# Kernel tuning notes

Hardware: AMD Instinct MI355X
Metric: run time of the kernel (lower is better)

## Reference

```python
import jax, jax.numpy as jnp
import numpy as np

DIM = 512
HEADS = 16
DIM_HEAD = 64
INNER = HEADS * DIM_HEAD
MAX_T = 32
BASE = 10000.0


def rotate_half(t):
    t1, t2 = jnp.split(t, 2, axis=-1)
    return jnp.concatenate((-t2, t1), axis=-1)


def setup_inputs() -> dict:
    key = jax.random.key(0)
    ks = jax.random.split(key, 12)
    B, T, S = 2, 16, 128
    x = jax.random.normal(ks[0], (B, T, S, DIM), dtype=jnp.float32)
    y = jax.random.normal(ks[1], (B, T, S, DIM), dtype=jnp.float32)
    temporal_mask = jax.random.randint(ks[2], (B, T, T), 0, 2).astype(jnp.int32)
    sc = 1.0 / np.sqrt(DIM)
    Wq = jax.random.normal(ks[3], (DIM, INNER), dtype=jnp.float32) * sc
    Wk = jax.random.normal(ks[4], (DIM, INNER), dtype=jnp.float32) * sc
    Wv = jax.random.normal(ks[5], (DIM, INNER), dtype=jnp.float32) * sc
    Wo = jax.random.normal(ks[6], (INNER, DIM), dtype=jnp.float32) / np.sqrt(INNER)
    bo = jnp.zeros((DIM,), dtype=jnp.float32)
    pos_emb = jax.random.normal(ks[7], (MAX_T, DIM), dtype=jnp.float32)
    gate_w = jax.random.normal(ks[8], (DIM, 1), dtype=jnp.float32) * sc
    gate_b = jnp.zeros((1,), dtype=jnp.float32)
    return {"x": x, "y": y, "temporal_mask": temporal_mask, "Wq": Wq, "Wk": Wk,
            "Wv": Wv, "Wo": Wo, "bo": bo, "pos_emb": pos_emb,
            "gate_w": gate_w, "gate_b": gate_b}


def reference(x, y, temporal_mask, Wq, Wk, Wv, Wo, bo, pos_emb, gate_w, gate_b):
    B, T, S, D = x.shape
    n = T * S
    scale = DIM_HEAD ** (-0.5)
    # temporal positional embedding (T <= MAX_T path)
    tp = pos_emb[:T][None, :, None, :]  # [1,T,1,D]
    x = x + tp
    y = y + tp
    xf = x.reshape(B, n, D)
    yf = y.reshape(B, n, D)
    # NOTE: k is computed from x (as in the source), v from y
    q = (xf @ Wq).reshape(B, n, HEADS, DIM_HEAD).transpose(0, 2, 1, 3)
    k = (xf @ Wk).reshape(B, n, HEADS, DIM_HEAD).transpose(0, 2, 1, 3)
    v = (yf @ Wv).reshape(B, n, HEADS, DIM_HEAD).transpose(0, 2, 1, 3)
    # RoPE over flattened token index
    inv_freq = 1.0 / (BASE ** (jnp.arange(0, DIM_HEAD, 2, dtype=jnp.float32) / DIM_HEAD))
    freqs = jnp.arange(n, dtype=jnp.float32)[:, None] * inv_freq[None, :]  # [n, d/2]
    emb = jnp.concatenate((freqs, freqs), axis=-1)  # [n, d]
    fc = jnp.cos(emb)[None, None, :, :]
    fs = jnp.sin(emb)[None, None, :, :]
    q = q * fc + rotate_half(q) * fs
    k = k * fc + rotate_half(k) * fs
    dots = jnp.einsum('bhid,bhjd->bhij', q, k) * scale  # [B,H,n,n]
    # expand temporal mask [B,T,T] -> [B,1,n,n] block structure
    m = jnp.repeat(jnp.repeat(temporal_mask, S, axis=1), S, axis=2)[:, None, :, :]
    dots = jnp.where(m == 0, -jnp.inf, dots)
    attn = jax.nn.softmax(dots, axis=-1)
    out = jnp.einsum('bhij,bhjd->bhid', attn, v)  # [B,H,n,d]
    out = out.transpose(0, 2, 1, 3).reshape(B, n, INNER)
    out = out @ Wo + bo
    out = out.reshape(B, T, S, D)
    gate = jax.nn.sigmoid(out @ gate_w + gate_b)  # [B,T,S,1]
    return out * gate
```

## Files before the change

kernel.cpp:

```cpp
#include <hip/hip_runtime.h>
#include <hip/hip_bf16.h>

typedef __attribute__((ext_vector_type(4))) short short4v;
typedef __attribute__((ext_vector_type(8))) short short8v;
typedef __attribute__((ext_vector_type(4))) float float4v;
typedef __attribute__((ext_vector_type(2))) unsigned int uint2v;
typedef __attribute__((ext_vector_type(4))) unsigned int uint4v;

#define NTOK 2048
#define MROWS 4096
#define DMODEL 512
#define NINNER 1024
#define DH 64
#define HH 16
#define LOG2E 1.4426950408889634f

__device__ __forceinline__ unsigned short b2s(float f) {
    __hip_bfloat16 h = __float2bfloat16(f);
    return __builtin_bit_cast(unsigned short, h);
}
__device__ __forceinline__ float bf2f(unsigned short h) {
    unsigned int u = ((unsigned int)h) << 16;
    return __builtin_bit_cast(float, u);
}

__device__ __forceinline__ float4v mfma32(short8v a, short8v b, float4v c) {
    return __builtin_amdgcn_mfma_f32_16x16x32_bf16(a, b, c, 0, 0, 0);
}

__device__ __forceinline__ void gld16(const void* g, void* l) {
    __builtin_amdgcn_global_load_lds((const __attribute__((address_space(1))) void*)g,
                                     (__attribute__((address_space(3))) void*)l, 16, 0, 0);
}

__global__ void k_pre(const float* __restrict__ x, const float* __restrict__ y,
                      const float* __restrict__ pe,
                      unsigned short* __restrict__ xpb, unsigned short* __restrict__ ypb,
                      const float* __restrict__ Wq, const float* __restrict__ Wk,
                      const float* __restrict__ Wv, const float* __restrict__ Wo,
                      const float* __restrict__ gwv, const float* __restrict__ gbv,
                      const float* __restrict__ bo,
                      unsigned short* __restrict__ wall, unsigned short* __restrict__ wot,
                      float* __restrict__ ctab, float* __restrict__ stab,
                      unsigned short* __restrict__ gvp, float* __restrict__ bgp) {
    __shared__ float tl[64][65];
    const int blk = blockIdx.x;
    const int tid = threadIdx.x;
    if (blk < 2048) {
        int e0 = (blk * 256 + tid) * 4;
        int row = e0 >> 9, col = e0 & 511;
        int t = (row & (NTOK - 1)) >> 7;
        const float4v xv = *(const float4v*)(x + e0);
        const float4v yv = *(const float4v*)(y + e0);
        const float4v pv = *(const float4v*)(pe + t * DMODEL + col);
        short4v xo, yo;
#pragma unroll
        for (int i = 0; i < 4; ++i) {
            xo[i] = (short)b2s(xv[i] + pv[i]);
            yo[i] = (short)b2s(yv[i] + pv[i]);
        }
        *(short4v*)(xpb + e0) = xo;
        *(short4v*)(ypb + e0) = yo;
    } else if (blk < 2560) {
        int t = blk - 2048;
        const float* W;
        unsigned short* dst;
        int K, N, k0, n0;
        if (t < 384) {
            int which = t / 128, tile = t % 128;
            W = (which == 0) ? Wq : (which == 1) ? Wk : Wv;
            dst = wall + (size_t)which * 1024 * 512;
            K = 512; N = 1024;
            k0 = (tile >> 4) * 64; n0 = (tile & 15) * 64;
        } else {
            int tile = t - 384;
            W = Wo; dst = wot;
            K = 1024; N = 512;
            k0 = (tile >> 3) * 64; n0 = (tile & 7) * 64;
        }
        int tx = tid & 63, ty4 = tid >> 6;
#pragma unroll
        for (int p = 0; p < 16; ++p) {
            int ky = p * 4 + ty4;
            tl[ky][tx] = W[(size_t)(k0 + ky) * N + n0 + tx];
        }
        __syncthreads();
#pragma unroll
        for (int p = 0; p < 16; ++p) {
            int ny = p * 4 + ty4;
            dst[(size_t)(n0 + ny) * K + k0 + tx] = b2s(tl[tx][ny]);
        }
    } else if (blk < 2816) {
        int idx = (blk - 2560) * 256 + tid;
        int p = idx >> 5, j = idx & 31;
        float invf = powf(10000.0f, -(float)(2 * j) * (1.0f / 64.0f));
        float f = (float)p * invf;
        ctab[idx] = cosf(f);
        stab[idx] = sinf(f);
    } else if (blk < 2832) {
        int base = (blk - 2816) * 64;
        int w = tid >> 6, l = tid & 63, l16 = l & 15, g = l >> 4;
        int row = base + w * 16 + l16;
        const float* wr = Wo + (size_t)row * 512 + g * 128;
        const float* gr = gwv + g * 128;
        float s = 0.f;
#pragma unroll
        for (int t = 0; t < 32; ++t) {
            float4v a = *(const float4v*)(wr + t * 4);
            float4v b = *(const float4v*)(gr + t * 4);
            s += a[0] * b[0] + a[1] * b[1] + a[2] * b[2] + a[3] * b[3];
        }
        s += __shfl_xor(s, 16);
        s += __shfl_xor(s, 32);
        if (g == 0) gvp[row] = b2s(s);
    } else {
        if (tid < 64) {
            float s = 0.f;
#pragma unroll
            for (int t = 0; t < 8; ++t) s += bo[tid + t * 64] * gwv[tid + t * 64];
#pragma unroll
            for (int off = 32; off > 0; off >>= 1) s += __shfl_xor(s, off);
            if (tid == 0) bgp[0] = s + gbv[0];
        }
    }
}

__global__ __launch_bounds__(256) void k_qkv(const unsigned short* __restrict__ A,
                                             const unsigned short* __restrict__ A2,
                                             const unsigned short* __restrict__ Bt,
                                             unsigned short* __restrict__ Cq,
                                             unsigned short* __restrict__ Ck,
                                             unsigned short* __restrict__ Cvv,
                                             const float* __restrict__ ctab,
                                             const float* __restrict__ stab,
                                             float scale) {
    __shared__ unsigned short Ab[2][4096];
    __shared__ unsigned short Bb[2][4096];
    const int tid = threadIdx.x;
    const int w = tid >> 6, l = tid & 63, l16 = l & 15, g = l >> 4;
    const int wm = w >> 1, wn = w & 1;
    const int m0 = blockIdx.y * 128, n0 = blockIdx.x * 128;
    const unsigned short* Ap = (n0 >= 2048) ? A2 : A;
    float4v acc[4][4];
#pragma unroll
    for (int i = 0; i < 4; ++i)
#pragma unroll
        for (int j = 0; j < 4; ++j) acc[i][j] = (float4v){0.f, 0.f, 0.f, 0.f};

    auto stage = [&](int t, int buf) {
        int k0 = t * 32;
#pragma unroll
        for (int it = 0; it < 2; ++it) {
            int f = it * 4 + w;
            gld16(Ap + (size_t)(m0 + f * 16 + l16) * 512 + k0 + g * 8, &Ab[buf][f * 512]);
            gld16(Bt + (size_t)(n0 + f * 16 + l16) * 512 + k0 + g * 8, &Bb[buf][f * 512]);
        }
    };

    stage(0, 0);
    __syncthreads();
    for (int t = 0; t < 16; ++t) {
        const int cur = t & 1;
        if (t + 1 < 16) stage(t + 1, cur ^ 1);
        short8v af[4], bf[4];
#pragma unroll
        for (int mi = 0; mi < 4; ++mi)
            af[mi] = *(const short8v*)&Ab[cur][(wm * 4 + mi) * 512 + l * 8];
#pragma unroll
        for (int nj = 0; nj < 4; ++nj)
            bf[nj] = *(const short8v*)&Bb[cur][(wn * 4 + nj) * 512 + l * 8];
        __builtin_amdgcn_s_setprio(1);
#pragma unroll
        for (int mi = 0; mi < 4; ++mi)
#pragma unroll
            for (int nj = 0; nj < 4; ++nj)
                acc[mi][nj] = mfma32(af[mi], bf[nj], acc[mi][nj]);
        __builtin_amdgcn_s_setprio(0);
        __syncthreads();
    }

    const int hh = (n0 + wn * 64) >> 6;
    const int head = hh & 15;
    if (hh < 32) {
        unsigned short* out = (hh < 16) ? Cq : Ck;
        const float sc = (hh < 16) ? scale : 1.0f;
#pragma unroll
        for (int mi = 0; mi < 4; ++mi)
#pragma unroll
            for (int r = 0; r < 4; ++r) {
                int row = m0 + wm * 64 + mi * 16 + g * 4 + r;
                int b = row >> 11, pos = row & (NTOK - 1);
                const float* cr = ctab + pos * 32;
                const float* sr = stab + pos * 32;
                unsigned short* ob = out + (size_t)((b * HH + head) * NTOK + pos) * DH;
#pragma unroll
                for (int nj = 0; nj < 2; ++nj) {
                    int j = nj * 16 + l16;
                    float c = cr[j], s = sr[j];
                    float v1 = acc[mi][nj][r], v2 = acc[mi][nj + 2][r];
                    ob[j] = b2s((v1 * c - v2 * s) * sc);
                    ob[j + 32] = b2s((v2 * c + v1 * s) * sc);
                }
            }
    } else {
#pragma unroll
        for (int mi = 0; mi < 4; ++mi)
#pragma unroll
            for (int nj = 0; nj < 4; ++nj) {
                int d = nj * 16 + l16;
                int row0 = m0 + wm * 64 + mi * 16 + g * 4;
                int b = row0 >> 11, pos0 = row0 & (NTOK - 1);
                short4v o;
#pragma unroll
                for (int r = 0; r < 4; ++r) o[r] = (short)b2s(acc[mi][nj][r]);
                *(short4v*)(Cvv + (size_t)((b * HH + head) * DH + d) * NTOK + pos0) = o;
            }
    }
}

__global__ __launch_bounds__(256) void k_gatev(const unsigned short* __restrict__ otm,
                                               const unsigned short* __restrict__ gv,
                                               const float* __restrict__ bgp,
                                               float* __restrict__ glog) {
    int row = blockIdx.x * 4 + (threadIdx.x >> 6);
    int l = threadIdx.x & 63;
    const unsigned short* pr = otm + (size_t)row * NINNER;
    float acc = 0.f;
#pragma unroll
    for (int c = 0; c < 2; ++c) {
        short8v a = *(const short8v*)(pr + (c * 64 + l) * 8);
        short8v b = *(const short8v*)(gv + (c * 64 + l) * 8);
#pragma unroll
        for (int j = 0; j < 8; ++j)
            acc = fmaf(bf2f((unsigned short)a[j]), bf2f((unsigned short)b[j]), acc);
    }
#pragma unroll
    for (int off = 32; off > 0; off >>= 1) acc += __shfl_xor(acc, off);
    if (l == 0) glog[row] = 1.0f / (1.0f + __expf(-(acc + bgp[0])));
}

__global__ __launch_bounds__(256) void k_oproj(const unsigned short* __restrict__ A,
                                               const unsigned short* __restrict__ Bt,
                                               const float* __restrict__ bo,
                                               const float* __restrict__ glog,
                                               float* __restrict__ out) {
    __shared__ unsigned short Ab[2][2048];
    __shared__ unsigned short Bb[2][2048];
    const int tid = threadIdx.x;
    const int w = tid >> 6, l = tid & 63, l16 = l & 15, g = l >> 4;
    const int m0 = blockIdx.y * 64, n0 = blockIdx.x * 64;
    float4v acc[4];
#pragma unroll
    for (int j = 0; j < 4; ++j) acc[j] = (float4v){0.f, 0.f, 0.f, 0.f};

    auto stage = [&](int t, int buf) {
        int k0 = t * 32;
        gld16(A + (size_t)(m0 + w * 16 + l16) * 1024 + k0 + g * 8, &Ab[buf][w * 512]);
        gld16(Bt + (size_t)(n0 + w * 16 + l16) * 1024 + k0 + g * 8, &Bb[buf][w * 512]);
    };

    stage(0, 0);
    __syncthreads();
    for (int t = 0; t < 32; ++t) {
        const int cur = t & 1;
        if (t + 1 < 32) stage(t + 1, cur ^ 1);
        short8v af = *(const short8v*)&Ab[cur][w * 512 + l * 8];
        short8v bf[4];
#pragma unroll
        for (int nj = 0; nj < 4; ++nj)
            bf[nj] = *(const short8v*)&Bb[cur][nj * 512 + l * 8];
        __builtin_amdgcn_s_setprio(1);
#pragma unroll
        for (int nj = 0; nj < 4; ++nj)
            acc[nj] = mfma32(af, bf[nj], acc[nj]);
        __builtin_amdgcn_s_setprio(0);
        __syncthreads();
    }
    float gl[4];
#pragma unroll
    for (int r = 0; r < 4; ++r) gl[r] = glog[m0 + w * 16 + g * 4 + r];
#pragma unroll
    for (int nj = 0; nj < 4; ++nj) {
        int col = n0 + nj * 16 + l16;
        float bv = bo[col];
#pragma unroll
        for (int r = 0; r < 4; ++r) {
            int row = m0 + w * 16 + g * 4 + r;
            out[(size_t)row * 512 + col] = (acc[nj][r] + bv) * gl[r];
        }
    }
}

__global__ __launch_bounds__(512) void k_attn(const unsigned short* __restrict__ qh,
                                              const unsigned short* __restrict__ kh,
                                              const unsigned short* __restrict__ vt,
                                              const int* __restrict__ tmask,
                                              unsigned short* __restrict__ otmp) {
    __shared__ unsigned short Kb[3][4096];
    __shared__ unsigned short Vb[2][4096];
    __shared__ int tlist[33];
    const int blk = blockIdx.x;
    const int u = (blk & 7) * 64 + (blk >> 3);
    const int ti = u & 15, h = (u >> 4) & 15, b = u >> 8;
    const int tid = threadIdx.x, w = tid >> 6, l = tid & 63, l16 = l & 15, g = l >> 4;
    if (tid == 0) {
        int c = 0;
        for (int j = 0; j < 16; ++j)
            if (tmask[(b * 16 + ti) * 16 + j]) { tlist[c++] = 2 * j; tlist[c++] = 2 * j + 1; }
        tlist[32] = c;
    }
    __syncthreads();
    const int cnt = tlist[32];
    const unsigned short* qb = qh + (size_t)((b * HH + h) * NTOK) * DH;
    const unsigned short* kb = kh + (size_t)((b * HH + h) * NTOK) * DH;
    const unsigned short* vb = vt + (size_t)((b * HH + h) * DH) * NTOK;
    const int q0 = ti * 128 + w * 16;

    short8v qf[2];
#pragma unroll
    for (int c = 0; c < 2; ++c)
        qf[c] = *(const short8v*)(qb + (size_t)(q0 + l16) * DH + c * 32 + g * 8);

    short8v ones;
#pragma unroll
    for (int j = 0; j < 8; ++j) ones[j] = (short)0x3F80;

    float4v oacc[4];
#pragma unroll
    for (int i = 0; i < 4; ++i) oacc[i] = (float4v){0.f, 0.f, 0.f, 0.f};
    float4v lsum = (float4v){0.f, 0.f, 0.f, 0.f};
    float mx = -1e30f;
    uint4v vrg;
    float4v sA[4], sB[4];

    auto stageK = [&](int st, int buf) {
        const unsigned short* ga =
            kb + (size_t)(st * 64 + (w >> 1) * 16 + l16) * DH + (w & 1) * 32 + g * 8;
        gld16(ga, &Kb[buf][w * 512]);
    };
    auto loadV = [&](int st) {
        const unsigned short* ga =
            vb + (size_t)((w >> 1) * 16 + l16) * NTOK + st * 64 + (w & 1) * 32 + g * 4;
        uint2v lo = *(const uint2v*)ga;
        uint2v hi = *(const uint2v*)(ga + 16);
        vrg = (uint4v){lo[0], lo[1], hi[0], hi[1]};
    };
    auto writeV = [&](int buf) {
        *(uint4v*)&Vb[buf][w * 512 + l * 8] = vrg;
    };
    auto qkcomp = [&](int buf, float4v (&s)[4]) {
#pragma unroll
        for (int jk = 0; jk < 4; ++jk) s[jk] = (float4v){0.f, 0.f, 0.f, 0.f};
        __builtin_amdgcn_s_setprio(1);
#pragma unroll
        for (int jk = 0; jk < 4; ++jk) {
            short8v kf0 = *(const short8v*)&Kb[buf][(jk * 2 + 0) * 512 + l * 8];
            short8v kf1 = *(const short8v*)&Kb[buf][(jk * 2 + 1) * 512 + l * 8];
            s[jk] = mfma32(kf0, qf[0], s[jk]);
            s[jk] = mfma32(kf1, qf[1], s[jk]);
        }
        __builtin_amdgcn_s_setprio(0);
    };

    auto body = [&](int i, float4v (&scur)[4], float4v (&snext)[4]) {
        const bool pre1 = (i + 1 < cnt), pre2 = (i + 2 < cnt);
        if (pre2) stageK(tlist[i + 2], (i + 2) % 3);
        if (pre1) loadV(tlist[i + 1]);
        float tm = -1e30f;
#pragma unroll
        for (int jk = 0; jk < 4; ++jk) {
            float4v s4 = scur[jk];
            tm = fmaxf(tm, fmaxf(fmaxf(s4[0], s4[1]), fmaxf(s4[2], s4[3])));
        }
        tm = fmaxf(tm, __shfl_xor(tm, 16));
        tm = fmaxf(tm, __shfl_xor(tm, 32));
        if (!__all(tm <= mx + 8.0f)) {
            float mnew = fmaxf(mx, tm);
            float alpha = exp2f(mx - mnew);
#pragma unroll
            for (int r = 0; r < 4; ++r) lsum[r] *= alpha;
#pragma unroll
            for (int md = 0; md < 4; ++md)
#pragma unroll
                for (int r = 0; r < 4; ++r) oacc[md][r] *= alpha;
            mx = mnew;
        }
        if (pre1) qkcomp((i + 1) % 3, snext);
        short8v pf[2];
#pragma unroll
        for (int cc = 0; cc < 2; ++cc) {
            short8v pv;
#pragma unroll
            for (int r = 0; r < 4; ++r) {
                pv[r] = (short)b2s(exp2f(scur[2 * cc][r] - mx));
                pv[r + 4] = (short)b2s(exp2f(scur[2 * cc + 1][r] - mx));
            }
            pf[cc] = pv;
        }
        __builtin_amdgcn_s_setprio(1);
#pragma unroll
        for (int cc = 0; cc < 2; ++cc) lsum = mfma32(ones, pf[cc], lsum);
#pragma unroll
        for (int md = 0; md < 4; ++md)
#pragma unroll
            for (int cc = 0; cc < 2; ++cc) {
                short8v vf = *(const short8v*)&Vb[i & 1][(md * 2 + cc) * 512 + l * 8];
                oacc[md] = mfma32(vf, pf[cc], oacc[md]);
            }
        __builtin_amdgcn_s_setprio(0);
        if (pre1) writeV((i + 1) & 1);
        __syncthreads();
    };

    if (cnt > 0) {
        stageK(tlist[0], 0);
        loadV(tlist[0]);
        if (cnt > 1) stageK(tlist[1], 1);
        writeV(0);
        __syncthreads();
        qkcomp(0, sA);
        for (int i = 0; i < cnt; i += 2) {
            body(i, sA, sB);
            if (i + 1 < cnt) body(i + 1, sB, sA);
        }
    }
    float lrow = lsum[0];
    float inv = lrow > 0.f ? 1.0f / lrow : 0.f;
    int q = q0 + l16;
#pragma unroll
    for (int md = 0; md < 4; ++md) {
        short4v o;
#pragma unroll
        for (int r = 0; r < 4; ++r) o[r] = (short)b2s(oacc[md][r] * inv);
        *(short4v*)(otmp + (size_t)(b * NTOK + q) * NINNER + h * DH + md * 16 + g * 4) = o;
    }
}

extern "C" void kernel_launch(void* const* d_in, const int* in_sizes, int n_in,
                              void* d_out, int out_size, void* d_ws, size_t ws_size,
                              hipStream_t stream) {
    (void)in_sizes; (void)n_in; (void)out_size; (void)ws_size;
    const float* x = (const float*)d_in[0];
    const float* y = (const float*)d_in[1];
    const int* tmask = (const int*)d_in[2];
    const float* Wq = (const float*)d_in[3];
    const float* Wk = (const float*)d_in[4];
    const float* Wv = (const float*)d_in[5];
    const float* Wo = (const float*)d_in[6];
    const float* bo = (const float*)d_in[7];
    const float* pe = (const float*)d_in[8];
    const float* gw = (const float*)d_in[9];
    const float* gb = (const float*)d_in[10];

    char* ws = (char*)d_ws;
    const size_t MB = 1u << 20;
    unsigned short* xpb  = (unsigned short*)(ws + 0);
    unsigned short* ypb  = (unsigned short*)(ws + 4 * MB);
    unsigned short* wall = (unsigned short*)(ws + 8 * MB);
    unsigned short* wot  = (unsigned short*)(ws + 11 * MB);
    unsigned short* qh   = (unsigned short*)(ws + 12 * MB);
    unsigned short* kh   = (unsigned short*)(ws + 20 * MB);
    unsigned short* vt   = (unsigned short*)(ws + 28 * MB);
    unsigned short* otm  = (unsigned short*)(ws + 36 * MB);
    float* ct = (float*)(ws + 44 * MB);
    float* st = (float*)(ws + 44 * MB + 256 * 1024);
    unsigned short* gv = (unsigned short*)(ws + 45 * MB);
    float* bg = (float*)(ws + 45 * MB + 4096);
    float* glog = (float*)(ws + 45 * MB + 8192);
    float* outp = (float*)d_out;

    k_pre<<<2833, 256, 0, stream>>>(x, y, pe, xpb, ypb, Wq, Wk, Wv, Wo, gw, gb, bo,
                                    wall, wot, ct, st, gv, bg);
    k_qkv<<<dim3(24, 32), 256, 0, stream>>>(xpb, ypb, wall, qh, kh, vt, ct, st,
                                            0.125f * LOG2E);
    k_attn<<<512, 512, 0, stream>>>(qh, kh, vt, tmask, otm);
    k_gatev<<<1024, 256, 0, stream>>>(otm, gv, bg, glog);
    k_oproj<<<dim3(8, 64), 256, 0, stream>>>(otm, wot, bo, glog, outp);
}
```

Before: 117.7 us.

## Fuse gate dot-product into output projection and widen attention key tiles

Removes the separate gate kernel by computing the gate logit as an extra MFMA against the gate vector inside the output projection, using the same A fragments, and applying the sigmoid in the epilogue. The attention kernel now processes a full 128-key temporal block per iteration instead of 64-key sub-blocks, which halves loop iterations and barriers. It drops to double-buffered K, doubles the LDS and score registers, and adds a 4-blocks-per-CU launch bound. The gate is now computed redundantly in every column block of the projection.

```diff
diff --git a/kernel.cpp b/kernel.cpp
--- a/kernel.cpp
+++ b/kernel.cpp
@@ -218,31 +218,11 @@
     }
 }
 
-__global__ __launch_bounds__(256) void k_gatev(const unsigned short* __restrict__ otm,
-                                               const unsigned short* __restrict__ gv,
-                                               const float* __restrict__ bgp,
-                                               float* __restrict__ glog) {
-    int row = blockIdx.x * 4 + (threadIdx.x >> 6);
-    int l = threadIdx.x & 63;
-    const unsigned short* pr = otm + (size_t)row * NINNER;
-    float acc = 0.f;
-#pragma unroll
-    for (int c = 0; c < 2; ++c) {
-        short8v a = *(const short8v*)(pr + (c * 64 + l) * 8);
-        short8v b = *(const short8v*)(gv + (c * 64 + l) * 8);
-#pragma unroll
-        for (int j = 0; j < 8; ++j)
-            acc = fmaf(bf2f((unsigned short)a[j]), bf2f((unsigned short)b[j]), acc);
-    }
-#pragma unroll
-    for (int off = 32; off > 0; off >>= 1) acc += __shfl_xor(acc, off);
-    if (l == 0) glog[row] = 1.0f / (1.0f + __expf(-(acc + bgp[0])));
-}
-
 __global__ __launch_bounds__(256) void k_oproj(const unsigned short* __restrict__ A,
                                                const unsigned short* __restrict__ Bt,
                                                const float* __restrict__ bo,
-                                               const float* __restrict__ glog,
+                                               const unsigned short* __restrict__ gv,
+                                               const float* __restrict__ bgp,
                                                float* __restrict__ out) {
     __shared__ unsigned short Ab[2][2048];
     __shared__ unsigned short Bb[2][2048];
@@ -252,6 +232,7 @@
     float4v acc[4];
 #pragma unroll
     for (int j = 0; j < 4; ++j) acc[j] = (float4v){0.f, 0.f, 0.f, 0.f};
+    float4v gacc = (float4v){0.f, 0.f, 0.f, 0.f};
 
     auto stage = [&](int t, int buf) {
         int k0 = t * 32;
@@ -269,16 +250,19 @@
 #pragma unroll
         for (int nj = 0; nj < 4; ++nj)
             bf[nj] = *(const short8v*)&Bb[cur][nj * 512 + l * 8];
+        short8v gvf = *(const short8v*)(gv + t * 32 + g * 8);
         __builtin_amdgcn_s_setprio(1);
 #pragma unroll
         for (int nj = 0; nj < 4; ++nj)
             acc[nj] = mfma32(af, bf[nj], acc[nj]);
+        gacc = mfma32(af, gvf, gacc);
         __builtin_amdgcn_s_setprio(0);
         __syncthreads();
     }
+    const float bg = bgp[0];
     float gl[4];
 #pragma unroll
-    for (int r = 0; r < 4; ++r) gl[r] = glog[m0 + w * 16 + g * 4 + r];
+    for (int r = 0; r < 4; ++r) gl[r] = 1.0f / (1.0f + __expf(-(gacc[r] + bg)));
 #pragma unroll
     for (int nj = 0; nj < 4; ++nj) {
         int col = n0 + nj * 16 + l16;
@@ -291,14 +275,14 @@
     }
 }
 
-__global__ __launch_bounds__(512) void k_attn(const unsigned short* __restrict__ qh,
-                                              const unsigned short* __restrict__ kh,
-                                              const unsigned short* __restrict__ vt,
-                                              const int* __restrict__ tmask,
-                                              unsigned short* __restrict__ otmp) {
-    __shared__ unsigned short Kb[3][4096];
-    __shared__ unsigned short Vb[2][4096];
-    __shared__ int tlist[33];
+__global__ __launch_bounds__(512, 4) void k_attn(const unsigned short* __restrict__ qh,
+                                                 const unsigned short* __restrict__ kh,
+                                                 const unsigned short* __restrict__ vt,
+                                                 const int* __restrict__ tmask,
+                                                 unsigned short* __restrict__ otmp) {
+    __shared__ unsigned short Kb[2][8192];
+    __shared__ unsigned short Vb[2][8192];
+    __shared__ int tlist[17];
     const int blk = blockIdx.x;
     const int u = (blk & 7) * 64 + (blk >> 3);
     const int ti = u & 15, h = (u >> 4) & 15, b = u >> 8;
@@ -306,11 +290,11 @@
     if (tid == 0) {
         int c = 0;
         for (int j = 0; j < 16; ++j)
-            if (tmask[(b * 16 + ti) * 16 + j]) { tlist[c++] = 2 * j; tlist[c++] = 2 * j + 1; }
-        tlist[32] = c;
+            if (tmask[(b * 16 + ti) * 16 + j]) tlist[c++] = j;
+        tlist[16] = c;
     }
     __syncthreads();
-    const int cnt = tlist[32];
+    const int cnt = tlist[16];
     const unsigned short* qb = qh + (size_t)((b * HH + h) * NTOK) * DH;
     const unsigned short* kb = kh + (size_t)((b * HH + h) * NTOK) * DH;
     const unsigned short* vb = vt + (size_t)((b * HH + h) * DH) * NTOK;
@@ -330,30 +314,40 @@
     for (int i = 0; i < 4; ++i) oacc[i] = (float4v){0.f, 0.f, 0.f, 0.f};
     float4v lsum = (float4v){0.f, 0.f, 0.f, 0.f};
     float mx = -1e30f;
-    uint4v vrg;
-    float4v sA[4], sB[4];
-
-    auto stageK = [&](int st, int buf) {
-        const unsigned short* ga =
-            kb + (size_t)(st * 64 + (w >> 1) * 16 + l16) * DH + (w & 1) * 32 + g * 8;
-        gld16(ga, &Kb[buf][w * 512]);
-    };
-    auto loadV = [&](int st) {
-        const unsigned short* ga =
-            vb + (size_t)((w >> 1) * 16 + l16) * NTOK + st * 64 + (w & 1) * 32 + g * 4;
-        uint2v lo = *(const uint2v*)ga;
-        uint2v hi = *(const uint2v*)(ga + 16);
-        vrg = (uint4v){lo[0], lo[1], hi[0], hi[1]};
+    uint4v vrg[2];
+    float4v sA[8], sB[8];
+
+    auto stageK = [&](int tj, int buf) {
+#pragma unroll
+        for (int s = 0; s < 2; ++s) {
+            int fi = w * 2 + s;
+            const unsigned short* ga =
+                kb + (size_t)(tj * 128 + (fi >> 1) * 16 + l16) * DH + (fi & 1) * 32 + g * 8;
+            gld16(ga, &Kb[buf][fi * 512]);
+        }
+    };
+    auto loadV = [&](int tj) {
+#pragma unroll
+        for (int s = 0; s < 2; ++s) {
+            int fi = w * 2 + s;
+            const unsigned short* ga =
+                vb + (size_t)((fi >> 2) * 16 + l16) * NTOK + tj * 128 + (fi & 3) * 32 + g * 4;
+            uint2v lo = *(const uint2v*)ga;
+            uint2v hi = *(const uint2v*)(ga + 16);
+            vrg[s] = (uint4v){lo[0], lo[1], hi[0], hi[1]};
+        }
     };
     auto writeV = [&](int buf) {
-        *(uint4v*)&Vb[buf][w * 512 + l * 8] = vrg;
-    };
-    auto qkcomp = [&](int buf, float4v (&s)[4]) {
-#pragma unroll
-        for (int jk = 0; jk < 4; ++jk) s[jk] = (float4v){0.f, 0.f, 0.f, 0.f};
+#pragma unroll
+        for (int s = 0; s < 2; ++s)
+            *(uint4v*)&Vb[buf][(w * 2 + s) * 512 + l * 8] = vrg[s];
+    };
+    auto qkcomp = [&](int buf, float4v (&s)[8]) {
+#pragma unroll
+        for (int jk = 0; jk < 8; ++jk) s[jk] = (float4v){0.f, 0.f, 0.f, 0.f};
         __builtin_amdgcn_s_setprio(1);
 #pragma unroll
-        for (int jk = 0; jk < 4; ++jk) {
+        for (int jk = 0; jk < 8; ++jk) {
             short8v kf0 = *(const short8v*)&Kb[buf][(jk * 2 + 0) * 512 + l * 8];
             short8v kf1 = *(const short8v*)&Kb[buf][(jk * 2 + 1) * 512 + l * 8];
             s[jk] = mfma32(kf0, qf[0], s[jk]);
@@ -362,13 +356,13 @@
         __builtin_amdgcn_s_setprio(0);
     };
 
-    auto body = [&](int i, float4v (&scur)[4], float4v (&snext)[4]) {
+    auto body = [&](int i, float4v (&scur)[8], float4v (&snext)[8]) {
         const bool pre1 = (i + 1 < cnt), pre2 = (i + 2 < cnt);
-        if (pre2) stageK(tlist[i + 2], (i + 2) % 3);
+        if (pre2) stageK(tlist[i + 2], i & 1);
         if (pre1) loadV(tlist[i + 1]);
         float tm = -1e30f;
 #pragma unroll
-        for (int jk = 0; jk < 4; ++jk) {
+        for (int jk = 0; jk < 8; ++jk) {
             float4v s4 = scur[jk];
             tm = fmaxf(tm, fmaxf(fmaxf(s4[0], s4[1]), fmaxf(s4[2], s4[3])));
         }
@@ -385,10 +379,10 @@
                 for (int r = 0; r < 4; ++r) oacc[md][r] *= alpha;
             mx = mnew;
         }
-        if (pre1) qkcomp((i + 1) % 3, snext);
-        short8v pf[2];
-#pragma unroll
-        for (int cc = 0; cc < 2; ++cc) {
+        if (pre1) qkcomp((i + 1) & 1, snext);
+        short8v pf[4];
+#pragma unroll
+        for (int cc = 0; cc < 4; ++cc) {
             short8v pv;
 #pragma unroll
             for (int r = 0; r < 4; ++r) {
@@ -399,12 +393,12 @@
         }
         __builtin_amdgcn_s_setprio(1);
 #pragma unroll
-        for (int cc = 0; cc < 2; ++cc) lsum = mfma32(ones, pf[cc], lsum);
+        for (int cc = 0; cc < 4; ++cc) lsum = mfma32(ones, pf[cc], lsum);
 #pragma unroll
         for (int md = 0; md < 4; ++md)
 #pragma unroll
-            for (int cc = 0; cc < 2; ++cc) {
-                short8v vf = *(const short8v*)&Vb[i & 1][(md * 2 + cc) * 512 + l * 8];
+            for (int cc = 0; cc < 4; ++cc) {
+                short8v vf = *(const short8v*)&Vb[i & 1][(md * 4 + cc) * 512 + l * 8];
                 oacc[md] = mfma32(vf, pf[cc], oacc[md]);
             }
         __builtin_amdgcn_s_setprio(0);
@@ -466,7 +460,6 @@
     float* st = (float*)(ws + 44 * MB + 256 * 1024);
     unsigned short* gv = (unsigned short*)(ws + 45 * MB);
     float* bg = (float*)(ws + 45 * MB + 4096);
-    float* glog = (float*)(ws + 45 * MB + 8192);
     float* outp = (float*)d_out;
 
     k_pre<<<2833, 256, 0, stream>>>(x, y, pe, xpb, ypb, Wq, Wk, Wv, Wo, gw, gb, bo,
@@ -474,6 +467,5 @@
     k_qkv<<<dim3(24, 32), 256, 0, stream>>>(xpb, ypb, wall, qh, kh, vt, ct, st,
                                             0.125f * LOG2E);
     k_attn<<<512, 512, 0, stream>>>(qh, kh, vt, tmask, otm);
-    k_gatev<<<1024, 256, 0, stream>>>(otm, gv, bg, glog);
-    k_oproj<<<dim3(8, 64), 256, 0, stream>>>(otm, wot, bo, glog, outp);
-}
+    k_oproj<<<dim3(8, 64), 256, 0, stream>>>(otm, wot, bo, gv, bg, outp);
+}
```

After: 122.5 us. 1.04x slower.
